# Optimization experiments

Hardware: AMD Instinct MI355X
Metric: run time of the kernel (lower is better)

Reference implementation:

```python
import jax, jax.numpy as jnp
import numpy as np

RADIUS = 8
NUM = 200
EPS = 1e-8


def _conv2d(x, k, pad_mode):
    # x: [B,1,H,W], k: [kh,kw]; same-size conv with given numpy-style padding mode
    ph, pw = k.shape[0] // 2, k.shape[1] // 2
    xp = jnp.pad(x, ((0, 0), (0, 0), (ph, ph), (pw, pw)), mode=pad_mode)
    return jax.lax.conv_general_dilated(
        xp, k[None, None], (1, 1), 'VALID',
        dimension_numbers=('NCHW', 'OIHW', 'NCHW'))


def _gauss_kernel7():
    xs = np.arange(7, dtype=np.float32) - 3.0
    g = np.exp(-0.5 * xs ** 2)
    g /= g.sum()
    return jnp.asarray(np.outer(g, g))


def get_corners(imgs):
    B, _, H, W = imgs.shape
    # kornia rgb_to_grayscale
    gray = 0.299 * imgs[:, 0:1] + 0.587 * imgs[:, 1:2] + 0.114 * imgs[:, 2:3]
    # kornia CornerGFTT: sobel gradients (normalized), gaussian-smoothed structure tensor, min eigenvalue
    sob = jnp.array([[-1., 0., 1.], [-2., 0., 2.], [-1., 0., 1.]], jnp.float32) / 8.0
    dx = _conv2d(gray, sob, 'edge')
    dy = _conv2d(gray, sob.T, 'edge')
    g = _gauss_kernel7()
    dx2 = _conv2d(dx * dx, g, 'reflect')
    dy2 = _conv2d(dy * dy, g, 'reflect')
    dxy = _conv2d(dx * dy, g, 'reflect')
    tr = dx2 + dy2
    det = dx2 * dy2 - dxy * dxy
    resp = 0.5 * (tr - jnp.sqrt(jnp.abs(tr * tr - 4.0 * det)))  # GFTT score (min eigval)
    # kornia nms2d with 5x5 window: keep local maxima
    mp = jax.lax.reduce_window(resp, -jnp.inf, jax.lax.max,
                               (1, 1, 5, 5), (1, 1, 1, 1),
                               [(0, 0), (0, 0), (2, 2), (2, 2)])
    resp = jnp.where(resp == mp, resp, 0.0)
    # unfold/mask/fold with kernel=stride=RADIUS == per non-overlapping 8x8 block:
    # keep elements equal to the block max and > 0
    r = RADIUS
    blk = resp.reshape(B, 1, H // r, r, W // r, r)
    bmax = blk.max(axis=(3, 5), keepdims=True)
    blk = jnp.where((blk > 0) & (blk == bmax), blk, 0.0)
    corners = blk.reshape(B, H * W)
    # top-200 scatter then binarize
    vals, idx = jax.lax.top_k(corners, NUM)
    out = jnp.zeros_like(corners).at[jnp.arange(B)[:, None], idx].set(vals)
    return (out > 0).astype(imgs.dtype).reshape(B, 1, H, W)


def setup_inputs() -> dict:
    key = jax.random.key(0)
    k1, k2, k3, k4 = jax.random.split(key, 4)
    B, N, D, H, W = 16, 2048, 256, 384, 384
    return {
        'descriptors': jax.random.normal(k1, (B, N, D), jnp.float32),
        'scores': jax.random.uniform(k2, (B, N), jnp.float32),
        'scores_dense': jax.random.normal(k3, (B, 1, H, W), jnp.float32),
        'imgs': jax.random.uniform(k4, (B, 3, H, W), jnp.float32),
    }


def reference(descriptors, scores, scores_dense, imgs):
    corners = get_corners(imgs)
    # all-pairs cosine similarity within each batch: pcos[b,i,j]
    norms = jnp.linalg.norm(descriptors, axis=-1)  # [B,N]
    dots = jnp.einsum('bnd,bmd->bnm', descriptors, descriptors)
    pcos = dots / jnp.maximum(norms[:, :, None] * norms[:, None, :], EPS)
    # BCEWithLogitsLoss(scores_dense, corners), mean reduction
    bce = jnp.mean(jnp.logaddexp(0.0, scores_dense) - scores_dense * corners)
    return bce + jnp.mean(jax.nn.relu(pcos))
```

## Files before the change

### kernel.cpp

```cpp
#include <hip/hip_runtime.h>

#define H 384
#define W 384
#define HWSZ (H * W)
#define NB 16
#define ND 2048
#define DD 256

#define OFF_RESP  256
#define OFF_CVAL  9437440
#define OFF_CPOS  9584896
#define OFF_DESCB 9732352
#define OFF_INV   26509568
#define OFF_PSOFT 26640640
#define OFF_PGEMM 26643200
#define OFF_PCORN 26652160
#define OFF_CNT   26652224

__device__ __forceinline__ int clampi(int v) { return v < 0 ? 0 : (v > 383 ? 383 : v); }
__device__ __forceinline__ int refl(int v) { return v < 0 ? -v : (v >= 384 ? 766 - v : v); }

__device__ __forceinline__ unsigned f2e4m3(float x) {
  float a = fabsf(x);
  unsigned s = (__float_as_uint(x) >> 31) << 7;
  if (a >= 448.f) return s | 0x7E;
  if (a < 0.015625f) {
    int m = (int)rintf(a * 512.f);
    return s | (unsigned)m;
  }
  unsigned u = __float_as_uint(a);
  u += 0x7FFFF + ((u >> 20) & 1);
  unsigned e = (u >> 23) - 120;
  unsigned m = (u >> 20) & 7;
  return s | (e << 3) | m;
}

typedef float f32x4 __attribute__((ext_vector_type(4)));

__device__ __forceinline__ void load_lds16(const void* g, void* l) {
  __builtin_amdgcn_global_load_lds((const __attribute__((address_space(1))) void*)g,
                                   (__attribute__((address_space(3))) void*)l, 16, 0, 0);
}

__global__ __launch_bounds__(256) void stage1_kernel(const float* __restrict__ imgs,
                                                     float* __restrict__ resp,
                                                     const float* __restrict__ desc,
                                                     unsigned char* __restrict__ descF8,
                                                     float* __restrict__ invn) {
  __shared__ float pbuf[4448];
  __shared__ float ubuf[3648];
  float* p0 = pbuf;
  float* p1 = pbuf + 1482;
  float* p2 = pbuf + 2964;
  float* glf = ubuf;
  float* t0 = ubuf;
  float* t1 = ubuf + 1216;
  float* t2 = ubuf + 2432;

  if (blockIdx.x >= 2304) {
    int wave = threadIdx.x >> 6, lane = threadIdx.x & 63;
    int row = (blockIdx.x - 2304) * 4 + wave;
    const float4* src = (const float4*)(desc + (size_t)row * DD);
    float4 v = src[lane];
    unsigned pk = f2e4m3(v.x) | (f2e4m3(v.y) << 8) | (f2e4m3(v.z) << 16) | (f2e4m3(v.w) << 24);
    ((unsigned*)(descF8 + (size_t)row * DD))[lane] = pk;
    float ss = v.x * v.x + v.y * v.y + v.z * v.z + v.w * v.w;
    for (int off = 32; off; off >>= 1) ss += __shfl_down(ss, off, 64);
    if (lane == 0) invn[row] = 1.f / fmaxf(sqrtf(ss), 1e-4f);
    return;
  }

  const float GW[7] = {0.0044330482f, 0.0540055826f, 0.2420362294f, 0.3990502160f,
                       0.2420362294f, 0.0540055826f, 0.0044330482f};
  int bid = blockIdx.x;
  int b = bid / 144;
  int t = bid % 144;
  int Y0 = (t / 12) * 32, X0 = (t % 12) * 32;
  const float* ib = imgs + (size_t)b * 3 * HWSZ;

  for (int i = threadIdx.x; i < 1600; i += 256) {
    int r = i / 40, c = i % 40;
    int gy = clampi(Y0 - 4 + r), gx = clampi(X0 - 4 + c);
    const float* p = ib + gy * W + gx;
    glf[r * 41 + c] = 0.299f * p[0] + 0.587f * p[HWSZ] + 0.114f * p[2 * HWSZ];
  }
  __syncthreads();

  bool interior = (X0 >= 32 && X0 <= 320 && Y0 >= 32 && Y0 <= 320);

  if (interior) {
    for (int i = threadIdx.x; i < 1444; i += 256) {
      int r = i / 38, c = i % 38;
      const float* g0 = glf + r * 41 + c;
      float a = g0[0],  bb = g0[1],  cc = g0[2];
      float d = g0[41],              e = g0[43];
      float f = g0[82], g = g0[83],  h = g0[84];
      float dx = 0.125f * ((cc - a) + 2.f * (e - d) + (h - f));
      float dy = 0.125f * ((f - a) + 2.f * (g - bb) + (h - cc));
      p0[r * 39 + c] = dx * dx;
      p1[r * 39 + c] = dy * dy;
      p2[r * 39 + c] = dx * dy;
    }
  } else {
    for (int i = threadIdx.x; i < 1444; i += 256) {
      int r = i / 38, c = i % 38;
      int py = refl(Y0 - 3 + r), px = refl(X0 - 3 + c);
      int ym = clampi(py - 1) - (Y0 - 4), y0 = py - (Y0 - 4), yp = clampi(py + 1) - (Y0 - 4);
      int xm = clampi(px - 1) - (X0 - 4), x0 = px - (X0 - 4), xp = clampi(px + 1) - (X0 - 4);
      float a = glf[ym * 41 + xm], bb = glf[ym * 41 + x0], cc = glf[ym * 41 + xp];
      float d = glf[y0 * 41 + xm], e = glf[y0 * 41 + xp];
      float f = glf[yp * 41 + xm], g = glf[yp * 41 + x0], h = glf[yp * 41 + xp];
      float dx = 0.125f * ((cc - a) + 2.f * (e - d) + (h - f));
      float dy = 0.125f * ((f - a) + 2.f * (g - bb) + (h - cc));
      p0[r * 39 + c] = dx * dx;
      p1[r * 39 + c] = dy * dy;
      p2[r * 39 + c] = dx * dy;
    }
  }
  __syncthreads();

  for (int g = threadIdx.x; g < 304; g += 256) {
    int r = g >> 3, c0 = (g & 7) * 4;
    {
      float a[10];
#pragma unroll
      for (int dc = 0; dc < 10; dc++) a[dc] = p0[r * 39 + c0 + dc];
#pragma unroll
      for (int k = 0; k < 4; k++) {
        float sv = 0.f;
#pragma unroll
        for (int j = 0; j < 7; j++) sv += GW[j] * a[k + j];
        t0[r * 32 + c0 + k] = sv;
      }
    }
    {
      float a[10];
#pragma unroll
      for (int dc = 0; dc < 10; dc++) a[dc] = p1[r * 39 + c0 + dc];
#pragma unroll
      for (int k = 0; k < 4; k++) {
        float sv = 0.f;
#pragma unroll
        for (int j = 0; j < 7; j++) sv += GW[j] * a[k + j];
        t1[r * 32 + c0 + k] = sv;
      }
    }
    {
      float a[10];
#pragma unroll
      for (int dc = 0; dc < 10; dc++) a[dc] = p2[r * 39 + c0 + dc];
#pragma unroll
      for (int k = 0; k < 4; k++) {
        float sv = 0.f;
#pragma unroll
        for (int j = 0; j < 7; j++) sv += GW[j] * a[k + j];
        t2[r * 32 + c0 + k] = sv;
      }
    }
  }
  __syncthreads();

  {
    int r0 = (threadIdx.x >> 5) * 4, c = threadIdx.x & 31;
    float s0[4], s1[4], s2[4];
    {
      float a[10];
#pragma unroll
      for (int dr = 0; dr < 10; dr++) a[dr] = t0[(r0 + dr) * 32 + c];
#pragma unroll
      for (int k = 0; k < 4; k++) {
        float sv = 0.f;
#pragma unroll
        for (int j = 0; j < 7; j++) sv += GW[j] * a[k + j];
        s0[k] = sv;
      }
    }
    {
      float a[10];
#pragma unroll
      for (int dr = 0; dr < 10; dr++) a[dr] = t1[(r0 + dr) * 32 + c];
#pragma unroll
      for (int k = 0; k < 4; k++) {
        float sv = 0.f;
#pragma unroll
        for (int j = 0; j < 7; j++) sv += GW[j] * a[k + j];
        s1[k] = sv;
      }
    }
    {
      float a[10];
#pragma unroll
      for (int dr = 0; dr < 10; dr++) a[dr] = t2[(r0 + dr) * 32 + c];
#pragma unroll
      for (int k = 0; k < 4; k++) {
        float sv = 0.f;
#pragma unroll
        for (int j = 0; j < 7; j++) sv += GW[j] * a[k + j];
        s2[k] = sv;
      }
    }
#pragma unroll
    for (int k = 0; k < 4; k++) {
      float tr = s0[k] + s1[k];
      float det = s0[k] * s1[k] - s2[k] * s2[k];
      float disc = tr * tr - 4.f * det;
      float rv = 0.5f * (tr - sqrtf(fabsf(disc)));
      resp[(size_t)b * HWSZ + (Y0 + r0 + k) * W + (X0 + c)] = rv;
    }
  }
}

__global__ __launch_bounds__(256) void stage2_kernel(const float* __restrict__ resp,
                                                     float* __restrict__ cval,
                                                     unsigned* __restrict__ cpos,
                                                     const float4* __restrict__ sd4,
                                                     float* __restrict__ psoft,
                                                     const unsigned char* __restrict__ descF8,
                                                     const float* __restrict__ invn,
                                                     float* __restrict__ pgemm,
                                                     int* __restrict__ cnt3) {
  alignas(16) __shared__ char smem[35408];

  if (blockIdx.x < 2176) {
    char* lA = smem;
    char* lB = smem + 16384;
    float* r4 = (float*)(smem + 32768);

    int bx = blockIdx.x;
    bx = ((bx & 7) * 272) + (bx >> 3);
    int batch = bx / 136;
    int rem = bx % 136;
    int ti = 0, rowlen = 16;
    while (rem >= rowlen) { rem -= rowlen; rowlen--; ti++; }
    int tj = ti + rem;

    const unsigned char* Ab = descF8 + (size_t)batch * ND * DD;
    const float* inv = invn + batch * ND;
    int I0 = ti * 128, J0 = tj * 128;

    int tid = threadIdx.x;
    int wave = tid >> 6, lane = tid & 63;
    int rm = lane & 15, kq = lane >> 4;
    int wr = wave >> 1, wc = wave & 1;
    int lrow = lane >> 3;
    int lcolb = ((lane & 7) ^ lrow) << 4;
    int cx = rm & 7;

    f32x4 accf[4][4];
#pragma unroll
    for (int m = 0; m < 4; m++)
#pragma unroll
      for (int n = 0; n < 4; n++) accf[m][n] = (f32x4){0.f, 0.f, 0.f, 0.f};

    for (int k0 = 0; k0 < DD; k0 += 128) {
#pragma unroll
      for (int q = 0; q < 4; q++) {
        int chunk = wave * 4 + q;
        load_lds16(Ab + (size_t)(I0 + chunk * 8 + lrow) * DD + k0 + lcolb, lA + chunk * 1024);
        load_lds16(Ab + (size_t)(J0 + chunk * 8 + lrow) * DD + k0 + lcolb, lB + chunk * 1024);
      }
      __syncthreads();
#pragma unroll
      for (int kk = 0; kk < 128; kk += 32) {
        long af[4], bfr[4];
        int koff = kk + kq * 8;
        int pcol = ((((koff >> 4) ^ cx) << 4) | (koff & 8));
#pragma unroll
        for (int m = 0; m < 4; m++)
          af[m] = *reinterpret_cast<const long*>(lA + (wr * 64 + m * 16 + rm) * 128 + pcol);
#pragma unroll
        for (int n = 0; n < 4; n++)
          bfr[n] = *reinterpret_cast<const long*>(lB + (wc * 64 + n * 16 + rm) * 128 + pcol);
#pragma unroll
        for (int m = 0; m < 4; m++)
#pragma unroll
          for (int n = 0; n < 4; n++)
            accf[m][n] = __builtin_amdgcn_mfma_f32_16x16x32_fp8_fp8(af[m], bfr[n], accf[m][n], 0, 0, 0);
      }
      __syncthreads();
    }

    float wgt = (ti == tj) ? 1.f : 2.f;
    float invC[4];
#pragma unroll
    for (int n = 0; n < 4; n++) invC[n] = inv[J0 + wc * 64 + n * 16 + rm];
    float psum = 0.f;
#pragma unroll
    for (int m = 0; m < 4; m++) {
#pragma unroll
      for (int r = 0; r < 4; r++) {
        float invR = inv[I0 + wr * 64 + m * 16 + kq * 4 + r];
#pragma unroll
        for (int n = 0; n < 4; n++) psum += fmaxf(accf[m][n][r] * invR * invC[n], 0.f);
      }
    }
    psum *= wgt;
    for (int off = 32; off; off >>= 1) psum += __shfl_down(psum, off, 64);
    if (lane == 0) r4[wave] = psum;
    __syncthreads();
    if (tid == 0) pgemm[bx] = r4[0] + r4[1] + r4[2] + r4[3];
    return;
  }

  if (blockIdx.x >= 2752) {
    int sb = blockIdx.x - 2752;
    float* r4 = (float*)smem;
    if (sb == 0 && threadIdx.x == 0) *cnt3 = 0;
    float s = 0.f;
    int base = sb * 256 + threadIdx.x;
#pragma unroll
    for (int it = 0; it < 4; it++) {
      float4 v = sd4[base + it * 147456];
      s += fmaxf(v.x, 0.f) + log1pf(expf(-fabsf(v.x))) +
           fmaxf(v.y, 0.f) + log1pf(expf(-fabsf(v.y))) +
           fmaxf(v.z, 0.f) + log1pf(expf(-fabsf(v.z))) +
           fmaxf(v.w, 0.f) + log1pf(expf(-fabsf(v.w)));
    }
    for (int off = 32; off; off >>= 1) s += __shfl_down(s, off, 64);
    if ((threadIdx.x & 63) == 0) r4[threadIdx.x >> 6] = s;
    __syncthreads();
    if (threadIdx.x == 0) psoft[sb] = r4[0] + r4[1] + r4[2] + r4[3];
    return;
  }

  float (*rl)[69] = (float (*)[69])smem;
  float (*nl)[65] = (float (*)[65])(smem + 18768);

  int bid = blockIdx.x - 2176;
  int b = bid / 36;
  int t = bid % 36;
  int Y0 = (t / 6) * 64, X0 = (t % 6) * 64;
  const float* rb = resp + (size_t)b * HWSZ;

  for (int i = threadIdx.x; i < 68 * 68; i += 256) {
    int r = i / 68, c = i % 68;
    int gy = Y0 - 2 + r, gx = X0 - 2 + c;
    float v = -INFINITY;
    if (gy >= 0 && gy < H && gx >= 0 && gx < W) v = rb[gy * W + gx];
    rl[r][c] = v;
  }
  __syncthreads();

  for (int i = threadIdx.x; i < 4096; i += 256) {
    int r = i / 64, c = i % 64;
    float m = -INFINITY;
#pragma unroll
    for (int dr = 0; dr < 5; dr++)
#pragma unroll
      for (int dc = 0; dc < 5; dc++) m = fmaxf(m, rl[r + dr][c + dc]);
    float v = rl[r + 2][c + 2];
    nl[r][c] = (v == m) ? v : 0.f;
  }
  __syncthreads();

  if (threadIdx.x < 64) {
    int bi = threadIdx.x / 8, bj = threadIdx.x % 8;
    float bv = 0.f;
    unsigned bp = 0;
    for (int rr = 0; rr < 8; rr++)
      for (int cc = 0; cc < 8; cc++) {
        float v = nl[bi * 8 + rr][bj * 8 + cc];
        if (v > bv) { bv = v; bp = (unsigned)((Y0 + bi * 8 + rr) * W + (X0 + bj * 8 + cc)); }
      }
    int ci = b * 2304 + (Y0 / 8 + bi) * 48 + (X0 / 8 + bj);
    cval[ci] = bv;
    cpos[ci] = bp;
  }
}

__global__ __launch_bounds__(256) void stage3_kernel(const float* __restrict__ cval,
                                                     const unsigned* __restrict__ cpos,
                                                     const float* __restrict__ sd,
                                                     float* __restrict__ pcorn,
                                                     const float* __restrict__ psoft,
                                                     const float* __restrict__ pgemm,
                                                     int* __restrict__ cnt3,
                                                     float* __restrict__ out) {
  __shared__ int hist[256];
  __shared__ int pick[2];
  __shared__ unsigned eqpos[256];
  __shared__ int eqcnt;
  __shared__ int ri[4];
  __shared__ float r4[4];
  __shared__ int lastFlag;

  int b = blockIdx.x;
  int t = threadIdx.x;
  int lane = t & 63;

  unsigned bits[9], pos[9];
#pragma unroll
  for (int q = 0; q < 9; q++) {
    int i = t + q * 256;
    unsigned vb = 0, p = 0;
    if (i < 2304) {
      float v = cval[b * 2304 + i];
      if (v > 0.f) { vb = __float_as_uint(v); p = cpos[b * 2304 + i]; }
    }
    bits[q] = vb; pos[q] = p;
  }

  int P = 0;
#pragma unroll
  for (int q = 0; q < 9; q++) P += (bits[q] != 0u);
  for (int off = 32; off; off >>= 1) P += __shfl_down(P, off, 64);
  if (lane == 0) ri[t >> 6] = P;
  __syncthreads();
  int Ptot = ri[0] + ri[1] + ri[2] + ri[3];

  float total = 0.f;
  if (Ptot > 0) {
    int K = Ptot < 200 ? Ptot : 200;

    unsigned prefix = 0;
    int krem = K;
    for (int shift = 24; shift >= 0; shift -= 8) {
      hist[t] = 0;
      __syncthreads();
#pragma unroll
      for (int q = 0; q < 9; q++) {
        if (bits[q] != 0u &&
            (shift == 24 || (bits[q] >> (shift + 8)) == (prefix >> (shift + 8))))
          atomicAdd(&hist[(bits[q] >> shift) & 0xFF], 1);
      }
      __syncthreads();
      if (t < 64) {
        int h0 = hist[4 * t], h1 = hist[4 * t + 1], h2 = hist[4 * t + 2], h3 = hist[4 * t + 3];
        int tot = h0 + h1 + h2 + h3;
        int acc = tot;
        for (int d = 1; d < 64; d <<= 1) {
          int o = __shfl_down(acc, d, 64);
          if (t + d < 64) acc += o;
        }
        int excl = acc - tot;
        int G3 = excl, G2 = excl + h3, G1 = excl + h3 + h2, G0 = excl + h3 + h2 + h1;
        if (G0 < krem && G0 + h0 >= krem) { pick[0] = 4 * t;     pick[1] = G0; }
        if (G1 < krem && G1 + h1 >= krem) { pick[0] = 4 * t + 1; pick[1] = G1; }
        if (G2 < krem && G2 + h2 >= krem) { pick[0] = 4 * t + 2; pick[1] = G2; }
        if (G3 < krem && G3 + h3 >= krem) { pick[0] = 4 * t + 3; pick[1] = G3; }
      }
      __syncthreads();
      prefix |= ((unsigned)pick[0]) << shift;
      krem -= pick[1];
      __syncthreads();
    }

    if (t == 0) eqcnt = 0;
    __syncthreads();
    float s = 0.f;
#pragma unroll
    for (int q = 0; q < 9; q++) {
      if (bits[q] > prefix) s += sd[(size_t)b * HWSZ + pos[q]];
      else if (bits[q] != 0u && bits[q] == prefix) {
        int idx = atomicAdd(&eqcnt, 1);
        if (idx < 256) eqpos[idx] = pos[q];
      }
    }
    __syncthreads();
    int m = eqcnt;
    if (m <= krem) {
      if (t < m) s += sd[(size_t)b * HWSZ + eqpos[t]];
    } else {
      int mm = m < 256 ? m : 256;
      if (t < mm) {
        unsigned p = eqpos[t];
        int rank = 0;
        for (int u = 0; u < mm; u++) rank += (eqpos[u] < p);
        if (rank < krem) s += sd[(size_t)b * HWSZ + p];
      }
    }
    for (int off = 32; off; off >>= 1) s += __shfl_down(s, off, 64);
    if (lane == 0) r4[t >> 6] = s;
    __syncthreads();
    total = r4[0] + r4[1] + r4[2] + r4[3];
  }

  if (t == 0) {
    atomicExch(&pcorn[b], total);
    __threadfence();
    lastFlag = (atomicAdd(cnt3, 1) == 15);
  }
  __syncthreads();
  if (!lastFlag) return;

  float bce = 0.f;
  for (int i = t; i < 576; i += 256) bce += psoft[i];
  if (t < 16) bce -= atomicAdd(&pcorn[t], 0.f);
  float g = 0.f;
  for (int i = t; i < 2176; i += 256) g += pgemm[i];
  float v = bce * (1.f / 2359296.f) + g * (1.f / 67108864.f);
  for (int off = 32; off; off >>= 1) v += __shfl_down(v, off, 64);
  if (lane == 0) r4[t >> 6] = v;
  __syncthreads();
  if (t == 0) out[0] = r4[0] + r4[1] + r4[2] + r4[3];
}

extern "C" void kernel_launch(void* const* d_in, const int* in_sizes, int n_in,
                              void* d_out, int out_size, void* d_ws, size_t ws_size,
                              hipStream_t stream) {
  (void)in_sizes; (void)n_in; (void)out_size; (void)ws_size;
  const float* desc = (const float*)d_in[0];
  const float* sd = (const float*)d_in[2];
  const float* imgs = (const float*)d_in[3];
  float* out = (float*)d_out;

  char* w = (char*)d_ws;
  float* resp = (float*)(w + OFF_RESP);
  float* cval = (float*)(w + OFF_CVAL);
  unsigned* cpos = (unsigned*)(w + OFF_CPOS);
  unsigned char* descF8 = (unsigned char*)(w + OFF_DESCB);
  float* invn = (float*)(w + OFF_INV);
  float* psoft = (float*)(w + OFF_PSOFT);
  float* pgemm = (float*)(w + OFF_PGEMM);
  float* pcorn = (float*)(w + OFF_PCORN);
  int* cnt3 = (int*)(w + OFF_CNT);

  stage1_kernel<<<10496, 256, 0, stream>>>(imgs, resp, desc, descF8, invn);
  stage2_kernel<<<3328, 256, 0, stream>>>(resp, cval, cpos, (const float4*)sd, psoft,
                                          descF8, invn, pgemm, cnt3);
  stage3_kernel<<<16, 256, 0, stream>>>(cval, cpos, sd, pcorn, psoft, pgemm, cnt3, out);
}
```

Measured before the change: 168.5 us.

## Merge top-k stage into stage2 with spin-wait and move softplus to stage1

Moves the softplus reduction blocks from stage2 into stage1. Stage3 is folded into stage2 as 16 blocks that spin on per-batch NMS completion counters, and a last-block-done counter does the final reduction. NMS blocks are placed first so the top-k blocks can overlap with the GEMM blocks, removing one kernel launch and the tail of a serial 16-block kernel. The approach depends on the NMS blocks being scheduled before the spinning blocks, and it adds the cost of atomics and fences.

Result: slower. 227.8 us (+35.2%).

```diff
diff --git a/kernel.cpp b/kernel.cpp
--- a/kernel.cpp
+++ b/kernel.cpp
@@ -16,6 +16,7 @@
 #define OFF_PGEMM 26643200
 #define OFF_PCORN 26652160
 #define OFF_CNT   26652224
+#define OFF_NMSCNT 26652288
 
 __device__ __forceinline__ int clampi(int v) { return v < 0 ? 0 : (v > 383 ? 383 : v); }
 __device__ __forceinline__ int refl(int v) { return v < 0 ? -v : (v >= 384 ? 766 - v : v); }
@@ -46,7 +47,11 @@
                                                      float* __restrict__ resp,
                                                      const float* __restrict__ desc,
                                                      unsigned char* __restrict__ descF8,
-                                                     float* __restrict__ invn) {
+                                                     float* __restrict__ invn,
+                                                     const float4* __restrict__ sd4,
+                                                     float* __restrict__ psoft,
+                                                     int* __restrict__ cnt3,
+                                                     int* __restrict__ nmsCnt) {
   __shared__ float pbuf[4448];
   __shared__ float ubuf[3648];
   float* p0 = pbuf;
@@ -56,6 +61,30 @@
   float* t0 = ubuf;
   float* t1 = ubuf + 1216;
   float* t2 = ubuf + 2432;
+
+  if (blockIdx.x >= 10496) {
+    int sb = blockIdx.x - 10496;
+    float* r4 = pbuf;
+    if (sb == 0 && threadIdx.x < 17) {
+      if (threadIdx.x == 0) *cnt3 = 0;
+      else nmsCnt[threadIdx.x - 1] = 0;
+    }
+    float s = 0.f;
+    int base = sb * 256 + threadIdx.x;
+#pragma unroll
+    for (int it = 0; it < 4; it++) {
+      float4 v = sd4[base + it * 147456];
+      s += fmaxf(v.x, 0.f) + log1pf(expf(-fabsf(v.x))) +
+           fmaxf(v.y, 0.f) + log1pf(expf(-fabsf(v.y))) +
+           fmaxf(v.z, 0.f) + log1pf(expf(-fabsf(v.z))) +
+           fmaxf(v.w, 0.f) + log1pf(expf(-fabsf(v.w)));
+    }
+    for (int off = 32; off; off >>= 1) s += __shfl_down(s, off, 64);
+    if ((threadIdx.x & 63) == 0) r4[threadIdx.x >> 6] = s;
+    __syncthreads();
+    if (threadIdx.x == 0) psoft[sb] = r4[0] + r4[1] + r4[2] + r4[3];
+    return;
+  }
 
   if (blockIdx.x >= 2304) {
     int wave = threadIdx.x >> 6, lane = threadIdx.x & 63;
@@ -213,21 +242,181 @@
 __global__ __launch_bounds__(256) void stage2_kernel(const float* __restrict__ resp,
                                                      float* __restrict__ cval,
                                                      unsigned* __restrict__ cpos,
-                                                     const float4* __restrict__ sd4,
-                                                     float* __restrict__ psoft,
+                                                     const float* __restrict__ sd,
+                                                     const float* __restrict__ psoft,
                                                      const unsigned char* __restrict__ descF8,
                                                      const float* __restrict__ invn,
                                                      float* __restrict__ pgemm,
-                                                     int* __restrict__ cnt3) {
+                                                     float* __restrict__ pcorn,
+                                                     int* __restrict__ cnt3,
+                                                     int* __restrict__ nmsCnt,
+                                                     float* __restrict__ out) {
   alignas(16) __shared__ char smem[35408];
-
-  if (blockIdx.x < 2176) {
+  __shared__ int hist[256];
+  __shared__ int pick[2];
+  __shared__ unsigned eqpos[256];
+  __shared__ int eqcnt;
+  __shared__ int ri[4];
+  __shared__ float r4b[4];
+  __shared__ int finFlag;
+
+  int tid = threadIdx.x;
+
+  if (blockIdx.x < 576) {
+    float (*rl)[69] = (float (*)[69])smem;
+    float (*nl)[65] = (float (*)[65])(smem + 18768);
+
+    int bid = blockIdx.x;
+    int b = bid / 36;
+    int t = bid % 36;
+    int Y0 = (t / 6) * 64, X0 = (t % 6) * 64;
+    const float* rb = resp + (size_t)b * HWSZ;
+
+    for (int i = tid; i < 68 * 68; i += 256) {
+      int r = i / 68, c = i % 68;
+      int gy = Y0 - 2 + r, gx = X0 - 2 + c;
+      float v = -INFINITY;
+      if (gy >= 0 && gy < H && gx >= 0 && gx < W) v = rb[gy * W + gx];
+      rl[r][c] = v;
+    }
+    __syncthreads();
+
+    for (int i = tid; i < 4096; i += 256) {
+      int r = i / 64, c = i % 64;
+      float m = -INFINITY;
+#pragma unroll
+      for (int dr = 0; dr < 5; dr++)
+#pragma unroll
+        for (int dc = 0; dc < 5; dc++) m = fmaxf(m, rl[r + dr][c + dc]);
+      float v = rl[r + 2][c + 2];
+      nl[r][c] = (v == m) ? v : 0.f;
+    }
+    __syncthreads();
+
+    if (tid < 64) {
+      int bi = tid / 8, bj = tid % 8;
+      float bv = 0.f;
+      unsigned bp = 0;
+      for (int rr = 0; rr < 8; rr++)
+        for (int cc = 0; cc < 8; cc++) {
+          float v = nl[bi * 8 + rr][bj * 8 + cc];
+          if (v > bv) { bv = v; bp = (unsigned)((Y0 + bi * 8 + rr) * W + (X0 + bj * 8 + cc)); }
+        }
+      int ci = b * 2304 + (Y0 / 8 + bi) * 48 + (X0 / 8 + bj);
+      __hip_atomic_store(&cval[ci], bv, __ATOMIC_RELAXED, __HIP_MEMORY_SCOPE_AGENT);
+      __hip_atomic_store(&cpos[ci], bp, __ATOMIC_RELAXED, __HIP_MEMORY_SCOPE_AGENT);
+    }
+    __threadfence();
+    __syncthreads();
+    if (tid == 0) atomicAdd(&nmsCnt[b], 1);
+    return;
+  }
+
+  if (blockIdx.x < 592) {
+    int b = blockIdx.x - 576;
+    int t = tid;
+    int lane = t & 63;
+
+    if (t == 0) {
+      while (__hip_atomic_load(&nmsCnt[b], __ATOMIC_RELAXED, __HIP_MEMORY_SCOPE_AGENT) < 36)
+        __builtin_amdgcn_s_sleep(8);
+    }
+    __syncthreads();
+
+    unsigned bits[9], pos[9];
+#pragma unroll
+    for (int q = 0; q < 9; q++) {
+      int i = t + q * 256;
+      float v = __hip_atomic_load(&cval[b * 2304 + i], __ATOMIC_RELAXED, __HIP_MEMORY_SCOPE_AGENT);
+      unsigned p = __hip_atomic_load(&cpos[b * 2304 + i], __ATOMIC_RELAXED, __HIP_MEMORY_SCOPE_AGENT);
+      unsigned vb = 0, pp = 0;
+      if (v > 0.f) { vb = __float_as_uint(v); pp = p; }
+      bits[q] = vb; pos[q] = pp;
+    }
+
+    int P = 0;
+#pragma unroll
+    for (int q = 0; q < 9; q++) P += (bits[q] != 0u);
+    for (int off = 32; off; off >>= 1) P += __shfl_down(P, off, 64);
+    if (lane == 0) ri[t >> 6] = P;
+    __syncthreads();
+    int Ptot = ri[0] + ri[1] + ri[2] + ri[3];
+
+    float total = 0.f;
+    if (Ptot > 0) {
+      int K = Ptot < 200 ? Ptot : 200;
+
+      unsigned prefix = 0;
+      int krem = K;
+      for (int shift = 24; shift >= 0; shift -= 8) {
+        hist[t] = 0;
+        __syncthreads();
+#pragma unroll
+        for (int q = 0; q < 9; q++) {
+          if (bits[q] != 0u &&
+              (shift == 24 || (bits[q] >> (shift + 8)) == (prefix >> (shift + 8))))
+            atomicAdd(&hist[(bits[q] >> shift) & 0xFF], 1);
+        }
+        __syncthreads();
+        if (t < 64) {
+          int h0 = hist[4 * t], h1 = hist[4 * t + 1], h2 = hist[4 * t + 2], h3 = hist[4 * t + 3];
+          int tot = h0 + h1 + h2 + h3;
+          int acc = tot;
+          for (int d = 1; d < 64; d <<= 1) {
+            int o = __shfl_down(acc, d, 64);
+            if (t + d < 64) acc += o;
+          }
+          int excl = acc - tot;
+          int G3 = excl, G2 = excl + h3, G1 = excl + h3 + h2, G0 = excl + h3 + h2 + h1;
+          if (G0 < krem && G0 + h0 >= krem) { pick[0] = 4 * t;     pick[1] = G0; }
+          if (G1 < krem && G1 + h1 >= krem) { pick[0] = 4 * t + 1; pick[1] = G1; }
+          if (G2 < krem && G2 + h2 >= krem) { pick[0] = 4 * t + 2; pick[1] = G2; }
+          if (G3 < krem && G3 + h3 >= krem) { pick[0] = 4 * t + 3; pick[1] = G3; }
+        }
+        __syncthreads();
+        prefix |= ((unsigned)pick[0]) << shift;
+        krem -= pick[1];
+        __syncthreads();
+      }
+
+      if (t == 0) eqcnt = 0;
+      __syncthreads();
+      float s = 0.f;
+#pragma unroll
+      for (int q = 0; q < 9; q++) {
+        if (bits[q] > prefix) s += sd[(size_t)b * HWSZ + pos[q]];
+        else if (bits[q] != 0u && bits[q] == prefix) {
+          int idx = atomicAdd(&eqcnt, 1);
+          if (idx < 256) eqpos[idx] = pos[q];
+        }
+      }
+      __syncthreads();
+      int m = eqcnt;
+      if (m <= krem) {
+        if (t < m) s += sd[(size_t)b * HWSZ + eqpos[t]];
+      } else {
+        int mm = m < 256 ? m : 256;
+        if (t < mm) {
+          unsigned p = eqpos[t];
+          int rank = 0;
+          for (int u = 0; u < mm; u++) rank += (eqpos[u] < p);
+          if (rank < krem) s += sd[(size_t)b * HWSZ + p];
+        }
+      }
+      for (int off = 32; off; off >>= 1) s += __shfl_down(s, off, 64);
+      if (lane == 0) r4b[t >> 6] = s;
+      __syncthreads();
+      total = r4b[0] + r4b[1] + r4b[2] + r4b[3];
+    }
+
+    if (t == 0) atomicExch(&pcorn[b], total);
+  } else {
     char* lA = smem;
     char* lB = smem + 16384;
     float* r4 = (float*)(smem + 32768);
 
-    int bx = blockIdx.x;
-    bx = ((bx & 7) * 272) + (bx >> 3);
+    int bxl = blockIdx.x - 592;
+    int bx = ((bxl & 7) * 272) + (bxl >> 3);
     int batch = bx / 136;
     int rem = bx % 136;
     int ti = 0, rowlen = 16;
@@ -238,7 +427,6 @@
     const float* inv = invn + batch * ND;
     int I0 = ti * 128, J0 = tj * 128;
 
-    int tid = threadIdx.x;
     int wave = tid >> 6, lane = tid & 63;
     int rm = lane & 15, kq = lane >> 4;
     int wr = wave >> 1, wc = wave & 1;
@@ -298,201 +486,30 @@
     for (int off = 32; off; off >>= 1) psum += __shfl_down(psum, off, 64);
     if (lane == 0) r4[wave] = psum;
     __syncthreads();
-    if (tid == 0) pgemm[bx] = r4[0] + r4[1] + r4[2] + r4[3];
-    return;
-  }
-
-  if (blockIdx.x >= 2752) {
-    int sb = blockIdx.x - 2752;
-    float* r4 = (float*)smem;
-    if (sb == 0 && threadIdx.x == 0) *cnt3 = 0;
-    float s = 0.f;
-    int base = sb * 256 + threadIdx.x;
-#pragma unroll
-    for (int it = 0; it < 4; it++) {
-      float4 v = sd4[base + it * 147456];
-      s += fmaxf(v.x, 0.f) + log1pf(expf(-fabsf(v.x))) +
-           fmaxf(v.y, 0.f) + log1pf(expf(-fabsf(v.y))) +
-           fmaxf(v.z, 0.f) + log1pf(expf(-fabsf(v.z))) +
-           fmaxf(v.w, 0.f) + log1pf(expf(-fabsf(v.w)));
-    }
-    for (int off = 32; off; off >>= 1) s += __shfl_down(s, off, 64);
-    if ((threadIdx.x & 63) == 0) r4[threadIdx.x >> 6] = s;
-    __syncthreads();
-    if (threadIdx.x == 0) psoft[sb] = r4[0] + r4[1] + r4[2] + r4[3];
-    return;
-  }
-
-  float (*rl)[69] = (float (*)[69])smem;
-  float (*nl)[65] = (float (*)[65])(smem + 18768);
-
-  int bid = blockIdx.x - 2176;
-  int b = bid / 36;
-  int t = bid % 36;
-  int Y0 = (t / 6) * 64, X0 = (t % 6) * 64;
-  const float* rb = resp + (size_t)b * HWSZ;
-
-  for (int i = threadIdx.x; i < 68 * 68; i += 256) {
-    int r = i / 68, c = i % 68;
-    int gy = Y0 - 2 + r, gx = X0 - 2 + c;
-    float v = -INFINITY;
-    if (gy >= 0 && gy < H && gx >= 0 && gx < W) v = rb[gy * W + gx];
-    rl[r][c] = v;
+    if (tid == 0)
+      __hip_atomic_store(&pgemm[bx], r4[0] + r4[1] + r4[2] + r4[3],
+                         __ATOMIC_RELAXED, __HIP_MEMORY_SCOPE_AGENT);
+  }
+
+  if (tid == 0) {
+    __threadfence();
+    finFlag = (atomicAdd(cnt3, 1) == 2191);
   }
   __syncthreads();
-
-  for (int i = threadIdx.x; i < 4096; i += 256) {
-    int r = i / 64, c = i % 64;
-    float m = -INFINITY;
-#pragma unroll
-    for (int dr = 0; dr < 5; dr++)
-#pragma unroll
-      for (int dc = 0; dc < 5; dc++) m = fmaxf(m, rl[r + dr][c + dc]);
-    float v = rl[r + 2][c + 2];
-    nl[r][c] = (v == m) ? v : 0.f;
-  }
-  __syncthreads();
-
-  if (threadIdx.x < 64) {
-    int bi = threadIdx.x / 8, bj = threadIdx.x % 8;
-    float bv = 0.f;
-    unsigned bp = 0;
-    for (int rr = 0; rr < 8; rr++)
-      for (int cc = 0; cc < 8; cc++) {
-        float v = nl[bi * 8 + rr][bj * 8 + cc];
-        if (v > bv) { bv = v; bp = (unsigned)((Y0 + bi * 8 + rr) * W + (X0 + bj * 8 + cc)); }
-      }
-    int ci = b * 2304 + (Y0 / 8 + bi) * 48 + (X0 / 8 + bj);
-    cval[ci] = bv;
-    cpos[ci] = bp;
-  }
-}
-
-__global__ __launch_bounds__(256) void stage3_kernel(const float* __restrict__ cval,
-                                                     const unsigned* __restrict__ cpos,
-                                                     const float* __restrict__ sd,
-                                                     float* __restrict__ pcorn,
-                                                     const float* __restrict__ psoft,
-                                                     const float* __restrict__ pgemm,
-                                                     int* __restrict__ cnt3,
-                                                     float* __restrict__ out) {
-  __shared__ int hist[256];
-  __shared__ int pick[2];
-  __shared__ unsigned eqpos[256];
-  __shared__ int eqcnt;
-  __shared__ int ri[4];
-  __shared__ float r4[4];
-  __shared__ int lastFlag;
-
-  int b = blockIdx.x;
-  int t = threadIdx.x;
-  int lane = t & 63;
-
-  unsigned bits[9], pos[9];
-#pragma unroll
-  for (int q = 0; q < 9; q++) {
-    int i = t + q * 256;
-    unsigned vb = 0, p = 0;
-    if (i < 2304) {
-      float v = cval[b * 2304 + i];
-      if (v > 0.f) { vb = __float_as_uint(v); p = cpos[b * 2304 + i]; }
-    }
-    bits[q] = vb; pos[q] = p;
-  }
-
-  int P = 0;
-#pragma unroll
-  for (int q = 0; q < 9; q++) P += (bits[q] != 0u);
-  for (int off = 32; off; off >>= 1) P += __shfl_down(P, off, 64);
-  if (lane == 0) ri[t >> 6] = P;
-  __syncthreads();
-  int Ptot = ri[0] + ri[1] + ri[2] + ri[3];
-
-  float total = 0.f;
-  if (Ptot > 0) {
-    int K = Ptot < 200 ? Ptot : 200;
-
-    unsigned prefix = 0;
-    int krem = K;
-    for (int shift = 24; shift >= 0; shift -= 8) {
-      hist[t] = 0;
-      __syncthreads();
-#pragma unroll
-      for (int q = 0; q < 9; q++) {
-        if (bits[q] != 0u &&
-            (shift == 24 || (bits[q] >> (shift + 8)) == (prefix >> (shift + 8))))
-          atomicAdd(&hist[(bits[q] >> shift) & 0xFF], 1);
-      }
-      __syncthreads();
-      if (t < 64) {
-        int h0 = hist[4 * t], h1 = hist[4 * t + 1], h2 = hist[4 * t + 2], h3 = hist[4 * t + 3];
-        int tot = h0 + h1 + h2 + h3;
-        int acc = tot;
-        for (int d = 1; d < 64; d <<= 1) {
-          int o = __shfl_down(acc, d, 64);
-          if (t + d < 64) acc += o;
-        }
-        int excl = acc - tot;
-        int G3 = excl, G2 = excl + h3, G1 = excl + h3 + h2, G0 = excl + h3 + h2 + h1;
-        if (G0 < krem && G0 + h0 >= krem) { pick[0] = 4 * t;     pick[1] = G0; }
-        if (G1 < krem && G1 + h1 >= krem) { pick[0] = 4 * t + 1; pick[1] = G1; }
-        if (G2 < krem && G2 + h2 >= krem) { pick[0] = 4 * t + 2; pick[1] = G2; }
-        if (G3 < krem && G3 + h3 >= krem) { pick[0] = 4 * t + 3; pick[1] = G3; }
-      }
-      __syncthreads();
-      prefix |= ((unsigned)pick[0]) << shift;
-      krem -= pick[1];
-      __syncthreads();
-    }
-
-    if (t == 0) eqcnt = 0;
-    __syncthreads();
-    float s = 0.f;
-#pragma unroll
-    for (int q = 0; q < 9; q++) {
-      if (bits[q] > prefix) s += sd[(size_t)b * HWSZ + pos[q]];
-      else if (bits[q] != 0u && bits[q] == prefix) {
-        int idx = atomicAdd(&eqcnt, 1);
-        if (idx < 256) eqpos[idx] = pos[q];
-      }
-    }
-    __syncthreads();
-    int m = eqcnt;
-    if (m <= krem) {
-      if (t < m) s += sd[(size_t)b * HWSZ + eqpos[t]];
-    } else {
-      int mm = m < 256 ? m : 256;
-      if (t < mm) {
-        unsigned p = eqpos[t];
-        int rank = 0;
-        for (int u = 0; u < mm; u++) rank += (eqpos[u] < p);
-        if (rank < krem) s += sd[(size_t)b * HWSZ + p];
-      }
-    }
-    for (int off = 32; off; off >>= 1) s += __shfl_down(s, off, 64);
-    if (lane == 0) r4[t >> 6] = s;
-    __syncthreads();
-    total = r4[0] + r4[1] + r4[2] + r4[3];
-  }
-
-  if (t == 0) {
-    atomicExch(&pcorn[b], total);
-    __threadfence();
-    lastFlag = (atomicAdd(cnt3, 1) == 15);
-  }
-  __syncthreads();
-  if (!lastFlag) return;
-
+  if (!finFlag) return;
+
+  int t = tid, lane = tid & 63;
   float bce = 0.f;
   for (int i = t; i < 576; i += 256) bce += psoft[i];
-  if (t < 16) bce -= atomicAdd(&pcorn[t], 0.f);
+  if (t < 16) bce -= __hip_atomic_load(&pcorn[t], __ATOMIC_RELAXED, __HIP_MEMORY_SCOPE_AGENT);
   float g = 0.f;
-  for (int i = t; i < 2176; i += 256) g += pgemm[i];
+  for (int i = t; i < 2176; i += 256)
+    g += __hip_atomic_load(&pgemm[i], __ATOMIC_RELAXED, __HIP_MEMORY_SCOPE_AGENT);
   float v = bce * (1.f / 2359296.f) + g * (1.f / 67108864.f);
   for (int off = 32; off; off >>= 1) v += __shfl_down(v, off, 64);
-  if (lane == 0) r4[t >> 6] = v;
+  if (lane == 0) r4b[t >> 6] = v;
   __syncthreads();
-  if (t == 0) out[0] = r4[0] + r4[1] + r4[2] + r4[3];
+  if (t == 0) out[0] = r4b[0] + r4b[1] + r4b[2] + r4b[3];
 }
 
 extern "C" void kernel_launch(void* const* d_in, const int* in_sizes, int n_in,
@@ -514,9 +531,10 @@
   float* pgemm = (float*)(w + OFF_PGEMM);
   float* pcorn = (float*)(w + OFF_PCORN);
   int* cnt3 = (int*)(w + OFF_CNT);
-
-  stage1_kernel<<<10496, 256, 0, stream>>>(imgs, resp, desc, descF8, invn);
-  stage2_kernel<<<3328, 256, 0, stream>>>(resp, cval, cpos, (const float4*)sd, psoft,
-                                          descF8, invn, pgemm, cnt3);
-  stage3_kernel<<<16, 256, 0, stream>>>(cval, cpos, sd, pcorn, psoft, pgemm, cnt3, out);
+  int* nmsCnt = (int*)(w + OFF_NMSCNT);
+
+  stage1_kernel<<<11072, 256, 0, stream>>>(imgs, resp, desc, descF8, invn,
+                                           (const float4*)sd, psoft, cnt3, nmsCnt);
+  stage2_kernel<<<2768, 256, 0, stream>>>(resp, cval, cpos, sd, psoft,
+                                          descF8, invn, pgemm, pcorn, cnt3, nmsCnt, out);
 }
```

## Rebalance stages: move softplus sum to stage1, NMS-first ordering, separable max

Applied to the files above, without the earlier changes.

Moves the softplus reduction blocks over scores_dense from stage2 into stage1, so they overlap with the image-gradient and descriptor-conversion work. In stage2, NMS blocks are now dispatched first and GEMM tiles after them. The 5x5 max filter becomes separable, a row max followed by a column max, and suppresses in place in the halo buffer. The goal is better load balance across the two big launches and fewer LDS reads in NMS. The trade-off is a slightly larger shared buffer and a different block dispatch order.

After: 172.2 us. +2.2%, slower.

```diff
diff --git a/kernel.cpp b/kernel.cpp
--- a/kernel.cpp
+++ b/kernel.cpp
@@ -46,7 +46,10 @@
                                                      float* __restrict__ resp,
                                                      const float* __restrict__ desc,
                                                      unsigned char* __restrict__ descF8,
-                                                     float* __restrict__ invn) {
+                                                     float* __restrict__ invn,
+                                                     const float4* __restrict__ sd4,
+                                                     float* __restrict__ psoft,
+                                                     int* __restrict__ cnt3) {
   __shared__ float pbuf[4448];
   __shared__ float ubuf[3648];
   float* p0 = pbuf;
@@ -56,6 +59,27 @@
   float* t0 = ubuf;
   float* t1 = ubuf + 1216;
   float* t2 = ubuf + 2432;
+
+  if (blockIdx.x >= 10496) {
+    int sb = blockIdx.x - 10496;
+    float* r4 = pbuf;
+    if (sb == 0 && threadIdx.x == 0) *cnt3 = 0;
+    float s = 0.f;
+    int base = sb * 256 + threadIdx.x;
+#pragma unroll
+    for (int it = 0; it < 4; it++) {
+      float4 v = sd4[base + it * 147456];
+      s += fmaxf(v.x, 0.f) + log1pf(expf(-fabsf(v.x))) +
+           fmaxf(v.y, 0.f) + log1pf(expf(-fabsf(v.y))) +
+           fmaxf(v.z, 0.f) + log1pf(expf(-fabsf(v.z))) +
+           fmaxf(v.w, 0.f) + log1pf(expf(-fabsf(v.w)));
+    }
+    for (int off = 32; off; off >>= 1) s += __shfl_down(s, off, 64);
+    if ((threadIdx.x & 63) == 0) r4[threadIdx.x >> 6] = s;
+    __syncthreads();
+    if (threadIdx.x == 0) psoft[sb] = r4[0] + r4[1] + r4[2] + r4[3];
+    return;
+  }
 
   if (blockIdx.x >= 2304) {
     int wave = threadIdx.x >> 6, lane = threadIdx.x & 63;
@@ -213,159 +237,146 @@
 __global__ __launch_bounds__(256) void stage2_kernel(const float* __restrict__ resp,
                                                      float* __restrict__ cval,
                                                      unsigned* __restrict__ cpos,
-                                                     const float4* __restrict__ sd4,
-                                                     float* __restrict__ psoft,
                                                      const unsigned char* __restrict__ descF8,
                                                      const float* __restrict__ invn,
-                                                     float* __restrict__ pgemm,
-                                                     int* __restrict__ cnt3) {
-  alignas(16) __shared__ char smem[35408];
-
-  if (blockIdx.x < 2176) {
-    char* lA = smem;
-    char* lB = smem + 16384;
-    float* r4 = (float*)(smem + 32768);
-
-    int bx = blockIdx.x;
-    bx = ((bx & 7) * 272) + (bx >> 3);
-    int batch = bx / 136;
-    int rem = bx % 136;
-    int ti = 0, rowlen = 16;
-    while (rem >= rowlen) { rem -= rowlen; rowlen--; ti++; }
-    int tj = ti + rem;
-
-    const unsigned char* Ab = descF8 + (size_t)batch * ND * DD;
-    const float* inv = invn + batch * ND;
-    int I0 = ti * 128, J0 = tj * 128;
-
-    int tid = threadIdx.x;
-    int wave = tid >> 6, lane = tid & 63;
-    int rm = lane & 15, kq = lane >> 4;
-    int wr = wave >> 1, wc = wave & 1;
-    int lrow = lane >> 3;
-    int lcolb = ((lane & 7) ^ lrow) << 4;
-    int cx = rm & 7;
-
-    f32x4 accf[4][4];
-#pragma unroll
-    for (int m = 0; m < 4; m++)
-#pragma unroll
-      for (int n = 0; n < 4; n++) accf[m][n] = (f32x4){0.f, 0.f, 0.f, 0.f};
-
-    for (int k0 = 0; k0 < DD; k0 += 128) {
-#pragma unroll
-      for (int q = 0; q < 4; q++) {
-        int chunk = wave * 4 + q;
-        load_lds16(Ab + (size_t)(I0 + chunk * 8 + lrow) * DD + k0 + lcolb, lA + chunk * 1024);
-        load_lds16(Ab + (size_t)(J0 + chunk * 8 + lrow) * DD + k0 + lcolb, lB + chunk * 1024);
-      }
-      __syncthreads();
-#pragma unroll
-      for (int kk = 0; kk < 128; kk += 32) {
-        long af[4], bfr[4];
-        int koff = kk + kq * 8;
-        int pcol = ((((koff >> 4) ^ cx) << 4) | (koff & 8));
-#pragma unroll
-        for (int m = 0; m < 4; m++)
-          af[m] = *reinterpret_cast<const long*>(lA + (wr * 64 + m * 16 + rm) * 128 + pcol);
+                                                     float* __restrict__ pgemm) {
+  alignas(16) __shared__ char smem[36448];
+
+  if (blockIdx.x < 576) {
+    float (*rl)[69] = (float (*)[69])smem;
+    float (*rmx)[65] = (float (*)[65])(smem + 18768);
+
+    int bid = blockIdx.x;
+    int b = bid / 36;
+    int t = bid % 36;
+    int Y0 = (t / 6) * 64, X0 = (t % 6) * 64;
+    const float* rb = resp + (size_t)b * HWSZ;
+
+    for (int i = threadIdx.x; i < 68 * 68; i += 256) {
+      int r = i / 68, c = i % 68;
+      int gy = Y0 - 2 + r, gx = X0 - 2 + c;
+      float v = -INFINITY;
+      if (gy >= 0 && gy < H && gx >= 0 && gx < W) v = rb[gy * W + gx];
+      rl[r][c] = v;
+    }
+    __syncthreads();
+
+    for (int i = threadIdx.x; i < 68 * 64; i += 256) {
+      int r = i / 64, c = i % 64;
+      float m = rl[r][c];
+      m = fmaxf(m, rl[r][c + 1]);
+      m = fmaxf(m, rl[r][c + 2]);
+      m = fmaxf(m, rl[r][c + 3]);
+      m = fmaxf(m, rl[r][c + 4]);
+      rmx[r][c] = m;
+    }
+    __syncthreads();
+
+    for (int i = threadIdx.x; i < 4096; i += 256) {
+      int r = i / 64, c = i % 64;
+      float m = rmx[r][c];
+      m = fmaxf(m, rmx[r + 1][c]);
+      m = fmaxf(m, rmx[r + 2][c]);
+      m = fmaxf(m, rmx[r + 3][c]);
+      m = fmaxf(m, rmx[r + 4][c]);
+      float v = rl[r + 2][c + 2];
+      rl[r + 2][c + 2] = (v == m) ? v : 0.f;
+    }
+    __syncthreads();
+
+    if (threadIdx.x < 64) {
+      int bi = threadIdx.x / 8, bj = threadIdx.x % 8;
+      float bv = 0.f;
+      unsigned bp = 0;
+      for (int rr = 0; rr < 8; rr++)
+        for (int cc = 0; cc < 8; cc++) {
+          float v = rl[bi * 8 + rr + 2][bj * 8 + cc + 2];
+          if (v > bv) { bv = v; bp = (unsigned)((Y0 + bi * 8 + rr) * W + (X0 + bj * 8 + cc)); }
+        }
+      int ci = b * 2304 + (Y0 / 8 + bi) * 48 + (X0 / 8 + bj);
+      cval[ci] = bv;
+      cpos[ci] = bp;
+    }
+    return;
+  }
+
+  char* lA = smem;
+  char* lB = smem + 16384;
+  float* r4 = (float*)(smem + 32768);
+
+  int bxl = blockIdx.x - 576;
+  int bx = ((bxl & 7) * 272) + (bxl >> 3);
+  int batch = bx / 136;
+  int rem = bx % 136;
+  int ti = 0, rowlen = 16;
+  while (rem >= rowlen) { rem -= rowlen; rowlen--; ti++; }
+  int tj = ti + rem;
+
+  const unsigned char* Ab = descF8 + (size_t)batch * ND * DD;
+  const float* inv = invn + batch * ND;
+  int I0 = ti * 128, J0 = tj * 128;
+
+  int tid = threadIdx.x;
+  int wave = tid >> 6, lane = tid & 63;
+  int rm = lane & 15, kq = lane >> 4;
+  int wr = wave >> 1, wc = wave & 1;
+  int lrow = lane >> 3;
+  int lcolb = ((lane & 7) ^ lrow) << 4;
+  int cx = rm & 7;
+
+  f32x4 accf[4][4];
+#pragma unroll
+  for (int m = 0; m < 4; m++)
+#pragma unroll
+    for (int n = 0; n < 4; n++) accf[m][n] = (f32x4){0.f, 0.f, 0.f, 0.f};
+
+  for (int k0 = 0; k0 < DD; k0 += 128) {
+#pragma unroll
+    for (int q = 0; q < 4; q++) {
+      int chunk = wave * 4 + q;
+      load_lds16(Ab + (size_t)(I0 + chunk * 8 + lrow) * DD + k0 + lcolb, lA + chunk * 1024);
+      load_lds16(Ab + (size_t)(J0 + chunk * 8 + lrow) * DD + k0 + lcolb, lB + chunk * 1024);
+    }
+    __syncthreads();
+#pragma unroll
+    for (int kk = 0; kk < 128; kk += 32) {
+      long af[4], bfr[4];
+      int koff = kk + kq * 8;
+      int pcol = ((((koff >> 4) ^ cx) << 4) | (koff & 8));
+#pragma unroll
+      for (int m = 0; m < 4; m++)
+        af[m] = *reinterpret_cast<const long*>(lA + (wr * 64 + m * 16 + rm) * 128 + pcol);
+#pragma unroll
+      for (int n = 0; n < 4; n++)
+        bfr[n] = *reinterpret_cast<const long*>(lB + (wc * 64 + n * 16 + rm) * 128 + pcol);
+#pragma unroll
+      for (int m = 0; m < 4; m++)
 #pragma unroll
         for (int n = 0; n < 4; n++)
-          bfr[n] = *reinterpret_cast<const long*>(lB + (wc * 64 + n * 16 + rm) * 128 + pcol);
-#pragma unroll
-        for (int m = 0; m < 4; m++)
-#pragma unroll
-          for (int n = 0; n < 4; n++)
-            accf[m][n] = __builtin_amdgcn_mfma_f32_16x16x32_fp8_fp8(af[m], bfr[n], accf[m][n], 0, 0, 0);
-      }
-      __syncthreads();
-    }
-
-    float wgt = (ti == tj) ? 1.f : 2.f;
-    float invC[4];
-#pragma unroll
-    for (int n = 0; n < 4; n++) invC[n] = inv[J0 + wc * 64 + n * 16 + rm];
-    float psum = 0.f;
-#pragma unroll
-    for (int m = 0; m < 4; m++) {
-#pragma unroll
-      for (int r = 0; r < 4; r++) {
-        float invR = inv[I0 + wr * 64 + m * 16 + kq * 4 + r];
-#pragma unroll
-        for (int n = 0; n < 4; n++) psum += fmaxf(accf[m][n][r] * invR * invC[n], 0.f);
-      }
-    }
-    psum *= wgt;
-    for (int off = 32; off; off >>= 1) psum += __shfl_down(psum, off, 64);
-    if (lane == 0) r4[wave] = psum;
-    __syncthreads();
-    if (tid == 0) pgemm[bx] = r4[0] + r4[1] + r4[2] + r4[3];
-    return;
-  }
-
-  if (blockIdx.x >= 2752) {
-    int sb = blockIdx.x - 2752;
-    float* r4 = (float*)smem;
-    if (sb == 0 && threadIdx.x == 0) *cnt3 = 0;
-    float s = 0.f;
-    int base = sb * 256 + threadIdx.x;
-#pragma unroll
-    for (int it = 0; it < 4; it++) {
-      float4 v = sd4[base + it * 147456];
-      s += fmaxf(v.x, 0.f) + log1pf(expf(-fabsf(v.x))) +
-           fmaxf(v.y, 0.f) + log1pf(expf(-fabsf(v.y))) +
-           fmaxf(v.z, 0.f) + log1pf(expf(-fabsf(v.z))) +
-           fmaxf(v.w, 0.f) + log1pf(expf(-fabsf(v.w)));
-    }
-    for (int off = 32; off; off >>= 1) s += __shfl_down(s, off, 64);
-    if ((threadIdx.x & 63) == 0) r4[threadIdx.x >> 6] = s;
-    __syncthreads();
-    if (threadIdx.x == 0) psoft[sb] = r4[0] + r4[1] + r4[2] + r4[3];
-    return;
-  }
-
-  float (*rl)[69] = (float (*)[69])smem;
-  float (*nl)[65] = (float (*)[65])(smem + 18768);
-
-  int bid = blockIdx.x - 2176;
-  int b = bid / 36;
-  int t = bid % 36;
-  int Y0 = (t / 6) * 64, X0 = (t % 6) * 64;
-  const float* rb = resp + (size_t)b * HWSZ;
-
-  for (int i = threadIdx.x; i < 68 * 68; i += 256) {
-    int r = i / 68, c = i % 68;
-    int gy = Y0 - 2 + r, gx = X0 - 2 + c;
-    float v = -INFINITY;
-    if (gy >= 0 && gy < H && gx >= 0 && gx < W) v = rb[gy * W + gx];
-    rl[r][c] = v;
-  }
-  __syncthreads();
-
-  for (int i = threadIdx.x; i < 4096; i += 256) {
-    int r = i / 64, c = i % 64;
-    float m = -INFINITY;
-#pragma unroll
-    for (int dr = 0; dr < 5; dr++)
-#pragma unroll
-      for (int dc = 0; dc < 5; dc++) m = fmaxf(m, rl[r + dr][c + dc]);
-    float v = rl[r + 2][c + 2];
-    nl[r][c] = (v == m) ? v : 0.f;
-  }
-  __syncthreads();
-
-  if (threadIdx.x < 64) {
-    int bi = threadIdx.x / 8, bj = threadIdx.x % 8;
-    float bv = 0.f;
-    unsigned bp = 0;
-    for (int rr = 0; rr < 8; rr++)
-      for (int cc = 0; cc < 8; cc++) {
-        float v = nl[bi * 8 + rr][bj * 8 + cc];
-        if (v > bv) { bv = v; bp = (unsigned)((Y0 + bi * 8 + rr) * W + (X0 + bj * 8 + cc)); }
-      }
-    int ci = b * 2304 + (Y0 / 8 + bi) * 48 + (X0 / 8 + bj);
-    cval[ci] = bv;
-    cpos[ci] = bp;
-  }
+          accf[m][n] = __builtin_amdgcn_mfma_f32_16x16x32_fp8_fp8(af[m], bfr[n], accf[m][n], 0, 0, 0);
+    }
+    __syncthreads();
+  }
+
+  float wgt = (ti == tj) ? 1.f : 2.f;
+  float invC[4];
+#pragma unroll
+  for (int n = 0; n < 4; n++) invC[n] = inv[J0 + wc * 64 + n * 16 + rm];
+  float psum = 0.f;
+#pragma unroll
+  for (int m = 0; m < 4; m++) {
+#pragma unroll
+    for (int r = 0; r < 4; r++) {
+      float invR = inv[I0 + wr * 64 + m * 16 + kq * 4 + r];
+#pragma unroll
+      for (int n = 0; n < 4; n++) psum += fmaxf(accf[m][n][r] * invR * invC[n], 0.f);
+    }
+  }
+  psum *= wgt;
+  for (int off = 32; off; off >>= 1) psum += __shfl_down(psum, off, 64);
+  if (lane == 0) r4[wave] = psum;
+  __syncthreads();
+  if (tid == 0) pgemm[bx] = r4[0] + r4[1] + r4[2] + r4[3];
 }
 
 __global__ __launch_bounds__(256) void stage3_kernel(const float* __restrict__ cval,
@@ -382,7 +393,7 @@
   __shared__ int eqcnt;
   __shared__ int ri[4];
   __shared__ float r4[4];
-  __shared__ int lastFlag;
+  __shared__ int finFlag;
 
   int b = blockIdx.x;
   int t = threadIdx.x;
@@ -478,14 +489,14 @@
   if (t == 0) {
     atomicExch(&pcorn[b], total);
     __threadfence();
-    lastFlag = (atomicAdd(cnt3, 1) == 15);
-  }
-  __syncthreads();
-  if (!lastFlag) return;
+    finFlag = (atomicAdd(cnt3, 1) == 15);
+  }
+  __syncthreads();
+  if (!finFlag) return;
 
   float bce = 0.f;
   for (int i = t; i < 576; i += 256) bce += psoft[i];
-  if (t < 16) bce -= atomicAdd(&pcorn[t], 0.f);
+  if (t < 16) bce -= __hip_atomic_load(&pcorn[t], __ATOMIC_RELAXED, __HIP_MEMORY_SCOPE_AGENT);
   float g = 0.f;
   for (int i = t; i < 2176; i += 256) g += pgemm[i];
   float v = bce * (1.f / 2359296.f) + g * (1.f / 67108864.f);
@@ -515,8 +526,8 @@
   float* pcorn = (float*)(w + OFF_PCORN);
   int* cnt3 = (int*)(w + OFF_CNT);
 
-  stage1_kernel<<<10496, 256, 0, stream>>>(imgs, resp, desc, descF8, invn);
-  stage2_kernel<<<3328, 256, 0, stream>>>(resp, cval, cpos, (const float4*)sd, psoft,
-                                          descF8, invn, pgemm, cnt3);
+  stage1_kernel<<<11072, 256, 0, stream>>>(imgs, resp, desc, descF8, invn,
+                                           (const float4*)sd, psoft, cnt3);
+  stage2_kernel<<<2752, 256, 0, stream>>>(resp, cval, cpos, descF8, invn, pgemm);
   stage3_kernel<<<16, 256, 0, stream>>>(cval, cpos, sd, pcorn, psoft, pgemm, cnt3, out);
 }
```
